# Kernel tuning notes

Hardware: AMD Instinct MI355X
Metric: run time of the kernel (lower is better)

## Reference

```python
import jax, jax.numpy as jnp
import numpy as np


def setup_inputs() -> dict:
    key = jax.random.key(0)
    k1, k2, k3 = jax.random.split(key, 3)
    B, IN, EXP, K = 1024, 1024, 40, 7
    OUT = IN * EXP  # 40960
    x = jax.random.normal(k1, (B, IN), dtype=jnp.float32)
    # fixed fan-in projection matrix: K nonzeros per output row
    vals = jax.random.uniform(k2, (OUT, K), dtype=jnp.float32)
    idx = jax.random.randint(k3, (OUT, K), 0, IN, dtype=jnp.int32)
    return {"x": x, "vals": vals, "idx": idx}


def reference(x, vals, idx):
    # y[b, o] = sum_k vals[o, k] * x[b, idx[o, k]]
    # equivalent to (W_sparse @ x.T).T with W in COO, fixed fan-in K.
    # Loop over the small fixed fan-in K (=7) to avoid a [B, OUT, K] intermediate.
    K = idx.shape[1]
    y = x[:, idx[:, 0]] * vals[:, 0][None, :]  # [B, OUT]
    for k in range(1, K):
        y = y + x[:, idx[:, k]] * vals[:, k][None, :]
    return y
```

## Files before the change

kernel.cpp:

```cpp
#include <hip/hip_runtime.h>
#include <hip/hip_fp16.h>

#define BATCH   1024
#define IN      1024
#define OUT     40960
#define KF      7
#define BT      8
#define NO      4
#define THREADS 256
#define OTILE   (THREADS * NO)
#define CHUNKS  (OUT / 64)

#define PV_BYTES  ((size_t)CHUNKS * KF * 64 * 4)
#define XPK_BYTES ((size_t)(BATCH / 8) * IN * 8 * 2)
#define PIDX_BYTES ((size_t)CHUNKS * KF * 64 * 2)


__global__ __launch_bounds__(THREADS)
void repack_kernel(const float* __restrict__ x, const float* __restrict__ vals,
                   const int* __restrict__ idx,
                   float* __restrict__ pvals, __half* __restrict__ xpk,
                   unsigned short* __restrict__ pidx)
{
    const int gid = blockIdx.x * THREADS + threadIdx.x;
    if (blockIdx.x < 512) {
        const int g = gid >> 10;
        const int i = gid & 1023;
        const float* xb = x + (size_t)g * 8 * IN + i;
        union { __half h[8]; float4 f; } u;
#pragma unroll
        for (int r = 0; r < 8; ++r) u.h[r] = __float2half_rn(xb[(size_t)r * IN]);
        *(float4*)&xpk[(size_t)gid * 8] = u.f;
    } else {
        const int t2 = gid - 512 * THREADS;
        const int c  = t2 / (KF * 64);
        const int r  = t2 % (KF * 64);
        const int k  = r >> 6;
        const int l  = r & 63;
        const size_t src = (size_t)(c * 64 + l) * KF + k;
        pvals[t2] = vals[src];
        pidx[t2]  = (unsigned short)(idx[src] << 4);
    }
}

__global__ __launch_bounds__(THREADS, 4)
void sparse_proj(const float* __restrict__ pvals, const __half* __restrict__ xpk,
                 const unsigned short* __restrict__ pidx, float* __restrict__ y)
{
    __shared__ __align__(16) __half xs[IN * BT];

    const int t     = threadIdx.x;
    const int b0    = blockIdx.y * BT;
    const int obase = blockIdx.x * OTILE + t;

    {
        const float4* src = (const float4*)(xpk + (size_t)blockIdx.y * IN * 8);
        float4* dst = (float4*)xs;
#pragma unroll
        for (int r = 0; r < 4; ++r) dst[t + r * THREADS] = src[t + r * THREADS];
    }
    __syncthreads();

    float acc[NO][BT];
#pragma unroll
    for (int no = 0; no < NO; ++no)
#pragma unroll
        for (int r = 0; r < BT; ++r) acc[no][r] = 0.0f;

    const int w    = t >> 6;
    const int lane = t & 63;

#pragma unroll
    for (int no = 0; no < NO; ++no) {
        const int c = blockIdx.x * 16 + no * 4 + w;
        const unsigned short* ipp = pidx  + (size_t)c * (KF * 64) + lane;
        const float*          vpp = pvals + (size_t)c * (KF * 64) + lane;
#pragma unroll
        for (int k = 0; k < KF; ++k) {
            const unsigned off = ipp[k * 64];
            const float v      = vpp[k * 64];
            const float4 g = *(const float4*)((const char*)xs + off);
            const __half2 h0 = *(const __half2*)&g.x;
            const __half2 h1 = *(const __half2*)&g.y;
            const __half2 h2 = *(const __half2*)&g.z;
            const __half2 h3 = *(const __half2*)&g.w;
            acc[no][0] = fmaf(v, __low2float(h0),  acc[no][0]);
            acc[no][1] = fmaf(v, __high2float(h0), acc[no][1]);
            acc[no][2] = fmaf(v, __low2float(h1),  acc[no][2]);
            acc[no][3] = fmaf(v, __high2float(h1), acc[no][3]);
            acc[no][4] = fmaf(v, __low2float(h2),  acc[no][4]);
            acc[no][5] = fmaf(v, __high2float(h2), acc[no][5]);
            acc[no][6] = fmaf(v, __low2float(h3),  acc[no][6]);
            acc[no][7] = fmaf(v, __high2float(h3), acc[no][7]);
        }
    }

#pragma unroll
    for (int r = 0; r < BT; ++r) {
        float* yr = y + (size_t)(b0 + r) * OUT;
#pragma unroll
        for (int no = 0; no < NO; ++no) {
            __builtin_nontemporal_store(acc[no][r], &yr[obase + no * THREADS]);
        }
    }
}

extern "C" void kernel_launch(void* const* d_in, const int* in_sizes, int n_in,
                              void* d_out, int out_size, void* d_ws, size_t ws_size,
                              hipStream_t stream) {
    const float* x    = (const float*)d_in[0];
    const float* vals = (const float*)d_in[1];
    const int*   idx  = (const int*)d_in[2];
    float*       y    = (float*)d_out;

    float*          pvals = (float*)d_ws;
    __half*         xpk   = (__half*)((char*)d_ws + PV_BYTES);
    unsigned short* pidx  = (unsigned short*)((char*)d_ws + PV_BYTES + XPK_BYTES);

    repack_kernel<<<dim3(512 + 1120), dim3(THREADS), 0, stream>>>(
        x, vals, idx, pvals, xpk, pidx);

    dim3 grid(OUT / OTILE, BATCH / BT);
    sparse_proj<<<grid, dim3(THREADS), 0, stream>>>(pvals, xpk, pidx, y);
}
```

Before: 177.4 us.

## Double batch tile to 16 rows and pack index/value metadata into uint2

Each block now stages two 8-row packed x slabs (32 KB of LDS) and processes 16 batch rows per output, so each index/value pair loaded from global memory is reused across twice as many rows. Index and value are interleaved into a single uint2 so one 8-byte load replaces two separate loads. Accumulators are now scoped per output group and stored right after that group finishes, which lowers peak register use, and the occupancy hint is raised to 5. The costs are double the LDS per block, which can limit resident blocks, and half as many blocks in the grid.

```diff
diff --git a/kernel.cpp b/kernel.cpp
--- a/kernel.cpp
+++ b/kernel.cpp
@@ -5,22 +5,20 @@
 #define IN      1024
 #define OUT     40960
 #define KF      7
-#define BT      8
+#define BT      16
 #define NO      4
 #define THREADS 256
 #define OTILE   (THREADS * NO)
 #define CHUNKS  (OUT / 64)
 
-#define PV_BYTES  ((size_t)CHUNKS * KF * 64 * 4)
-#define XPK_BYTES ((size_t)(BATCH / 8) * IN * 8 * 2)
-#define PIDX_BYTES ((size_t)CHUNKS * KF * 64 * 2)
+#define PMETA_BYTES ((size_t)CHUNKS * KF * 64 * 8)
+#define XPK_BYTES   ((size_t)(BATCH / 8) * IN * 8 * 2)
 
 
 __global__ __launch_bounds__(THREADS)
 void repack_kernel(const float* __restrict__ x, const float* __restrict__ vals,
                    const int* __restrict__ idx,
-                   float* __restrict__ pvals, __half* __restrict__ xpk,
-                   unsigned short* __restrict__ pidx)
+                   uint2* __restrict__ pmeta, __half* __restrict__ xpk)
 {
     const int gid = blockIdx.x * THREADS + threadIdx.x;
     if (blockIdx.x < 512) {
@@ -38,34 +36,30 @@
         const int k  = r >> 6;
         const int l  = r & 63;
         const size_t src = (size_t)(c * 64 + l) * KF + k;
-        pvals[t2] = vals[src];
-        pidx[t2]  = (unsigned short)(idx[src] << 4);
+        uint2 m;
+        m.x = (unsigned)(idx[src] << 4);
+        m.y = __float_as_uint(vals[src]);
+        pmeta[t2] = m;
     }
 }
 
-__global__ __launch_bounds__(THREADS, 4)
-void sparse_proj(const float* __restrict__ pvals, const __half* __restrict__ xpk,
-                 const unsigned short* __restrict__ pidx, float* __restrict__ y)
+__global__ __launch_bounds__(THREADS, 5)
+void sparse_proj(const uint2* __restrict__ pmeta, const __half* __restrict__ xpk,
+                 float* __restrict__ y)
 {
-    __shared__ __align__(16) __half xs[IN * BT];
+    __shared__ __align__(16) __half xs[2 * IN * 8];
 
     const int t     = threadIdx.x;
     const int b0    = blockIdx.y * BT;
     const int obase = blockIdx.x * OTILE + t;
 
     {
-        const float4* src = (const float4*)(xpk + (size_t)blockIdx.y * IN * 8);
+        const float4* src = (const float4*)(xpk + (size_t)blockIdx.y * 2 * IN * 8);
         float4* dst = (float4*)xs;
 #pragma unroll
-        for (int r = 0; r < 4; ++r) dst[t + r * THREADS] = src[t + r * THREADS];
+        for (int r = 0; r < 8; ++r) dst[t + r * THREADS] = src[t + r * THREADS];
     }
     __syncthreads();
-
-    float acc[NO][BT];
-#pragma unroll
-    for (int no = 0; no < NO; ++no)
-#pragma unroll
-        for (int r = 0; r < BT; ++r) acc[no][r] = 0.0f;
 
     const int w    = t >> 6;
     const int lane = t & 63;
@@ -73,34 +67,49 @@
 #pragma unroll
     for (int no = 0; no < NO; ++no) {
         const int c = blockIdx.x * 16 + no * 4 + w;
-        const unsigned short* ipp = pidx  + (size_t)c * (KF * 64) + lane;
-        const float*          vpp = pvals + (size_t)c * (KF * 64) + lane;
+        const uint2* mp = pmeta + (size_t)c * (KF * 64) + lane;
+
+        float acc[BT];
+#pragma unroll
+        for (int r = 0; r < BT; ++r) acc[r] = 0.0f;
+
 #pragma unroll
         for (int k = 0; k < KF; ++k) {
-            const unsigned off = ipp[k * 64];
-            const float v      = vpp[k * 64];
-            const float4 g = *(const float4*)((const char*)xs + off);
-            const __half2 h0 = *(const __half2*)&g.x;
-            const __half2 h1 = *(const __half2*)&g.y;
-            const __half2 h2 = *(const __half2*)&g.z;
-            const __half2 h3 = *(const __half2*)&g.w;
-            acc[no][0] = fmaf(v, __low2float(h0),  acc[no][0]);
-            acc[no][1] = fmaf(v, __high2float(h0), acc[no][1]);
-            acc[no][2] = fmaf(v, __low2float(h1),  acc[no][2]);
-            acc[no][3] = fmaf(v, __high2float(h1), acc[no][3]);
-            acc[no][4] = fmaf(v, __low2float(h2),  acc[no][4]);
-            acc[no][5] = fmaf(v, __high2float(h2), acc[no][5]);
-            acc[no][6] = fmaf(v, __low2float(h3),  acc[no][6]);
-            acc[no][7] = fmaf(v, __high2float(h3), acc[no][7]);
+            const uint2 m = mp[k * 64];
+            const unsigned off = m.x;
+            const float v = __uint_as_float(m.y);
+            const float4 g0 = *(const float4*)((const char*)xs + off);
+            const float4 g1 = *(const float4*)((const char*)xs + 16384 + off);
+            const __half2 a0 = *(const __half2*)&g0.x;
+            const __half2 a1 = *(const __half2*)&g0.y;
+            const __half2 a2 = *(const __half2*)&g0.z;
+            const __half2 a3 = *(const __half2*)&g0.w;
+            const __half2 b0h = *(const __half2*)&g1.x;
+            const __half2 b1h = *(const __half2*)&g1.y;
+            const __half2 b2h = *(const __half2*)&g1.z;
+            const __half2 b3h = *(const __half2*)&g1.w;
+            acc[0]  = fmaf(v, __low2float(a0),  acc[0]);
+            acc[1]  = fmaf(v, __high2float(a0), acc[1]);
+            acc[2]  = fmaf(v, __low2float(a1),  acc[2]);
+            acc[3]  = fmaf(v, __high2float(a1), acc[3]);
+            acc[4]  = fmaf(v, __low2float(a2),  acc[4]);
+            acc[5]  = fmaf(v, __high2float(a2), acc[5]);
+            acc[6]  = fmaf(v, __low2float(a3),  acc[6]);
+            acc[7]  = fmaf(v, __high2float(a3), acc[7]);
+            acc[8]  = fmaf(v, __low2float(b0h),  acc[8]);
+            acc[9]  = fmaf(v, __high2float(b0h), acc[9]);
+            acc[10] = fmaf(v, __low2float(b1h),  acc[10]);
+            acc[11] = fmaf(v, __high2float(b1h), acc[11]);
+            acc[12] = fmaf(v, __low2float(b2h),  acc[12]);
+            acc[13] = fmaf(v, __high2float(b2h), acc[13]);
+            acc[14] = fmaf(v, __low2float(b3h),  acc[14]);
+            acc[15] = fmaf(v, __high2float(b3h), acc[15]);
         }
-    }
 
+        const int o = obase + no * THREADS;
 #pragma unroll
-    for (int r = 0; r < BT; ++r) {
-        float* yr = y + (size_t)(b0 + r) * OUT;
-#pragma unroll
-        for (int no = 0; no < NO; ++no) {
-            __builtin_nontemporal_store(acc[no][r], &yr[obase + no * THREADS]);
+        for (int r = 0; r < BT; ++r) {
+            __builtin_nontemporal_store(acc[r], &y[(size_t)(b0 + r) * OUT + o]);
         }
     }
 }
@@ -113,13 +122,12 @@
     const int*   idx  = (const int*)d_in[2];
     float*       y    = (float*)d_out;
 
-    float*          pvals = (float*)d_ws;
-    __half*         xpk   = (__half*)((char*)d_ws + PV_BYTES);
-    unsigned short* pidx  = (unsigned short*)((char*)d_ws + PV_BYTES + XPK_BYTES);
+    uint2*  pmeta = (uint2*)d_ws;
+    __half* xpk   = (__half*)((char*)d_ws + PMETA_BYTES);
 
     repack_kernel<<<dim3(512 + 1120), dim3(THREADS), 0, stream>>>(
-        x, vals, idx, pvals, xpk, pidx);
+        x, vals, idx, pmeta, xpk);
 
     dim3 grid(OUT / OTILE, BATCH / BT);
-    sparse_proj<<<grid, dim3(THREADS), 0, stream>>>(pvals, xpk, pidx, y);
+    sparse_proj<<<grid, dim3(THREADS), 0, stream>>>(pmeta, xpk, y);
 }
```

After: 177.8 us. About the same (+0.2%).
